# Optimization experiments

Hardware: AMD Instinct MI355X
Metric: run time of the kernel (lower is better)

## Reference

```python
import jax, jax.numpy as jnp
import numpy as np

H_DIM = 1024
N_HEADS = 16
HEAD_D = H_DIM // N_HEADS  # 64


def setup_inputs() -> dict:
    key = jax.random.key(0)
    ks = jax.random.split(key, 10)
    B, T, C = 2, 2048, H_DIM
    init = 1.0 / np.sqrt(C)  # lecun_normal-scale stand-in
    src = jax.random.normal(ks[0], (B, T, C), dtype=jnp.float32)
    mask = jnp.ones((B, T), dtype=jnp.float32)  # unused when causal
    Wq = jax.random.normal(ks[1], (C, H_DIM), dtype=jnp.float32) * init
    Wk = jax.random.normal(ks[2], (C, H_DIM), dtype=jnp.float32) * init
    Wv = jax.random.normal(ks[3], (C, H_DIM), dtype=jnp.float32) * init
    Wo = jax.random.normal(ks[4], (H_DIM, H_DIM), dtype=jnp.float32) * init
    bq = jnp.zeros((H_DIM,), jnp.float32)
    bk = jnp.zeros((H_DIM,), jnp.float32)
    bv = jnp.zeros((H_DIM,), jnp.float32)
    bo = jnp.zeros((H_DIM,), jnp.float32)
    return {"src": src, "mask": mask, "Wq": Wq, "bq": bq, "Wk": Wk, "bk": bk,
            "Wv": Wv, "bv": bv, "Wo": Wo, "bo": bo}


def reference(src, mask, Wq, bq, Wk, bk, Wv, bv, Wo, bo):
    # MaskedCausalAttention forward, deterministic=True (dropout = identity),
    # use_causal_mask=True.
    B, T, C = src.shape
    N, D = N_HEADS, HEAD_D
    # q,k,v: [B, N, T, D]
    q = (src @ Wq + bq).reshape(B, T, N, D).transpose(0, 2, 1, 3)
    k = (src @ Wk + bk).reshape(B, T, N, D).transpose(0, 2, 1, 3)
    v = (src @ Wv + bv).reshape(B, T, N, D).transpose(0, 2, 1, 3)
    # scores: [B, N, T, T]
    scores = jnp.einsum('bntd,bnsd->bnts', q, k) / jnp.sqrt(jnp.float32(D))
    causal = jnp.tril(jnp.ones((T, T), dtype=bool))[None, None]
    scores = jnp.where(causal, scores, -jnp.inf)
    probs = jax.nn.softmax(scores, axis=-1)
    attn = jnp.einsum('bnts,bnsd->bntd', probs, v)  # [B, N, T, D]
    attn = attn.transpose(0, 2, 1, 3).reshape(B, T, N * D)
    return attn @ Wo + bo
```

## Files before the change

kernel.cpp:

```cpp
#include <hip/hip_runtime.h>
#include <hip/hip_bf16.h>

typedef __hip_bfloat16 bf16;
typedef __attribute__((ext_vector_type(8))) short short8;
typedef __attribute__((ext_vector_type(4))) float f32x4;

#define BATCH 2
#define SEQ   2048
#define HDIM  1024
#define NHEAD 16
#define DHEAD 64
#define MROWS (BATCH*SEQ)

#define QSCALE 0.18033688f
#define EXP2F(x) __builtin_amdgcn_exp2f(x)

static __device__ __forceinline__ short f2bs(float x) {
    __hip_bfloat16 h = (__hip_bfloat16)x;
    return *reinterpret_cast<short*>(&h);
}
static __device__ __forceinline__ unsigned int pk2(float a, float b) {
    __hip_bfloat162 h = __float22bfloat162_rn(make_float2(a, b));
    return *reinterpret_cast<unsigned int*>(&h);
}

static __device__ __forceinline__ void gload16(const void* g, void* l) {
    __builtin_amdgcn_global_load_lds(
        (const __attribute__((address_space(1))) unsigned int*)g,
        (__attribute__((address_space(3))) unsigned int*)l, 16, 0, 0);
}

__global__ __launch_bounds__(256) void prep1(const float* __restrict__ src,
        const float* __restrict__ Wq, const float* __restrict__ Wk,
        const float* __restrict__ Wv,
        short* __restrict__ Sb, short* __restrict__ WqkT,
        short* __restrict__ WvT)
{
    __shared__ float t[64][65];
    const int bx = blockIdx.x, tid = threadIdx.x;
    if (bx < 4096) {
        int i = bx * 256 + tid;
        float4 v = ((const float4*)src)[i];
        ushort4 o;
        o.x = (unsigned short)f2bs(v.x);
        o.y = (unsigned short)f2bs(v.y);
        o.z = (unsigned short)f2bs(v.z);
        o.w = (unsigned short)f2bs(v.w);
        ((ushort4*)Sb)[i] = o;
        return;
    }
    const int tb = bx - 4096;
    const int wsel = tb >> 8;
    const float* W = (wsel == 0) ? Wq : (wsel == 1) ? Wk : Wv;
    short* dst = (wsel < 2) ? WqkT : WvT;
    const int roff = (wsel < 2) ? wsel * 1024 : 0;
    const int t8 = tb & 255;
    const int n0 = (t8 & 15) * 64, k0 = (t8 >> 4) * 64;
#pragma unroll
    for (int i = 0; i < 16; i++) {
        int idx = tid + i * 256, r = idx >> 6, c = idx & 63;
        t[r][c] = W[(size_t)(k0 + r) * HDIM + n0 + c];
    }
    __syncthreads();
#pragma unroll
    for (int i = 0; i < 16; i++) {
        int idx = tid + i * 256, c = idx >> 6, r = idx & 63;
        dst[(size_t)(roff + n0 + c) * HDIM + k0 + r] = f2bs(t[r][c]);
    }
}

__global__ __launch_bounds__(256) void gemm_qk(const short* __restrict__ A,
        const short* __restrict__ Bt,
        const float* __restrict__ bq, const float* __restrict__ bk,
        short* __restrict__ Qout, short* __restrict__ Kout)
{
    __shared__ short As[16 * 512];
    __shared__ short Bs[16 * 512];
    const int tid = threadIdx.x, lane = tid & 63, w = tid >> 6;
    const int quad = lane >> 4, l15 = lane & 15;
    const int m0 = blockIdx.y * 128, n0 = blockIdx.x * 128;
    const int wr = w >> 1, wc = w & 1;

    const short* gsrc[8];
    short* ldst[8];
#pragma unroll
    for (int i = 0; i < 8; i++) {
        int u = w * 8 + i;
        if (u < 16) {
            int mi = u >> 1, kh = u & 1;
            gsrc[i] = A + (size_t)(m0 + mi * 16 + l15) * HDIM + kh * 32 + quad * 8;
            ldst[i] = &As[u * 512];
        } else {
            int v = u - 16, ni = v >> 1, kh = v & 1;
            gsrc[i] = Bt + (size_t)(n0 + ni * 16 + l15) * HDIM + kh * 32 + quad * 8;
            ldst[i] = &Bs[v * 512];
        }
    }

    f32x4 acc[4][4];
#pragma unroll
    for (int i = 0; i < 4; i++)
#pragma unroll
        for (int j = 0; j < 4; j++) acc[i][j] = (f32x4){0.f, 0.f, 0.f, 0.f};

    for (int kk = 0; kk < 16; ++kk) {
        if (kk) __syncthreads();
#pragma unroll
        for (int i = 0; i < 8; i++) {
            gload16(gsrc[i], ldst[i]);
            gsrc[i] += 64;
        }
        __syncthreads();

#pragma unroll
        for (int kh = 0; kh < 2; kh++) {
            short8 af[4], bfr[4];
#pragma unroll
            for (int mi = 0; mi < 4; mi++)
                af[mi] = *(const short8*)&As[((wr * 4 + mi) * 2 + kh) * 512 + lane * 8];
#pragma unroll
            for (int ni = 0; ni < 4; ni++)
                bfr[ni] = *(const short8*)&Bs[((wc * 4 + ni) * 2 + kh) * 512 + lane * 8];
#pragma unroll
            for (int mi = 0; mi < 4; mi++)
#pragma unroll
                for (int ni = 0; ni < 4; ni++)
                    acc[mi][ni] = __builtin_amdgcn_mfma_f32_16x16x32_bf16(
                                      af[mi], bfr[ni], acc[mi][ni], 0, 0, 0);
        }
    }

    const int region = n0 >> 10;
    const float* bias = region ? bk : bq;
    const float oscale = region ? 1.0f : QSCALE;
    short* C = region ? Kout : Qout;

#pragma unroll
    for (int mi = 0; mi < 4; mi++) {
        int mB = m0 + (wr * 4 + mi) * 16 + quad * 4;
#pragma unroll
        for (int ni = 0; ni < 4; ni++) {
            int nl = (n0 + (wc * 4 + ni) * 16 + l15) & 1023;
            float bb = bias[nl];
#pragma unroll
            for (int r = 0; r < 4; r++)
                C[(size_t)(mB + r) * HDIM + nl] =
                    f2bs((acc[mi][ni][r] + bb) * oscale);
        }
    }
}

__global__ __launch_bounds__(256) void gemm_v(const short* __restrict__ A,
        const short* __restrict__ Bt, const float* __restrict__ bv,
        short* __restrict__ Vtout)
{
    __shared__ short As[8 * 512];
    __shared__ short Bs[16 * 512];
    const int tid = threadIdx.x, lane = tid & 63, w = tid >> 6;
    const int quad = lane >> 4, l15 = lane & 15;
    const int m0 = blockIdx.y * 64, n0 = blockIdx.x * 128;
    const int wr = w >> 1, wc = w & 1;

    const short* gsrc[6];
    short* ldst[6];
#pragma unroll
    for (int i = 0; i < 6; i++) {
        int u = w * 6 + i;
        if (u < 8) {
            int mi = u >> 1, kh = u & 1;
            gsrc[i] = A + (size_t)(m0 + mi * 16 + l15) * HDIM + kh * 32 + quad * 8;
            ldst[i] = &As[u * 512];
        } else {
            int v = u - 8, ni = v >> 1, kh = v & 1;
            gsrc[i] = Bt + (size_t)(n0 + ni * 16 + l15) * HDIM + kh * 32 + quad * 8;
            ldst[i] = &Bs[v * 512];
        }
    }

    f32x4 acc[2][4];
#pragma unroll
    for (int i = 0; i < 2; i++)
#pragma unroll
        for (int j = 0; j < 4; j++) acc[i][j] = (f32x4){0.f, 0.f, 0.f, 0.f};

    for (int kk = 0; kk < 16; ++kk) {
        if (kk) __syncthreads();
#pragma unroll
        for (int i = 0; i < 6; i++) {
            gload16(gsrc[i], ldst[i]);
            gsrc[i] += 64;
        }
        __syncthreads();

#pragma unroll
        for (int kh = 0; kh < 2; kh++) {
            short8 af[2], bfr[4];
#pragma unroll
            for (int mi = 0; mi < 2; mi++)
                af[mi] = *(const short8*)&As[((wr * 2 + mi) * 2 + kh) * 512 + lane * 8];
#pragma unroll
            for (int ni = 0; ni < 4; ni++)
                bfr[ni] = *(const short8*)&Bs[((wc * 4 + ni) * 2 + kh) * 512 + lane * 8];
#pragma unroll
            for (int mi = 0; mi < 2; mi++)
#pragma unroll
                for (int ni = 0; ni < 4; ni++)
                    acc[mi][ni] = __builtin_amdgcn_mfma_f32_16x16x32_bf16(
                                      af[mi], bfr[ni], acc[mi][ni], 0, 0, 0);
        }
    }

#pragma unroll
    for (int mi = 0; mi < 2; mi++) {
        int mB = m0 + (wr * 2 + mi) * 16 + quad * 4;
        int bb = mB >> 11, t = mB & 2047;
#pragma unroll
        for (int ni = 0; ni < 4; ni++) {
            int n = n0 + (wc * 4 + ni) * 16 + l15;
            int h = n >> 6, d = n & 63;
            float bvv = bv[n];
            size_t base = ((size_t)((bb * NHEAD + h) * DHEAD + d)) * SEQ + t;
            ushort4 pk;
            pk.x = (unsigned short)f2bs(acc[mi][ni][0] + bvv);
            pk.y = (unsigned short)f2bs(acc[mi][ni][1] + bvv);
            pk.z = (unsigned short)f2bs(acc[mi][ni][2] + bvv);
            pk.w = (unsigned short)f2bs(acc[mi][ni][3] + bvv);
            *(ushort4*)(Vtout + base) = pk;
        }
    }
}

__global__ __launch_bounds__(256) void gemm_o(const short* __restrict__ A,
        const short* __restrict__ Bt, const float* __restrict__ bo,
        float* __restrict__ Out)
{
    __shared__ short As[8 * 512];
    __shared__ short Bs[16 * 512];
    const int tid = threadIdx.x, lane = tid & 63, w = tid >> 6;
    const int quad = lane >> 4, l15 = lane & 15;
    const int m0 = blockIdx.y * 64, n0 = blockIdx.x * 128;
    const int wr = w >> 1, wc = w & 1;

    const short* gsrc[6];
    short* ldst[6];
#pragma unroll
    for (int i = 0; i < 6; i++) {
        int u = w * 6 + i;
        if (u < 8) {
            int mi = u >> 1, kh = u & 1;
            gsrc[i] = A + (size_t)(m0 + mi * 16 + l15) * HDIM + kh * 32 + quad * 8;
            ldst[i] = &As[u * 512];
        } else {
            int v = u - 8, ni = v >> 1, kh = v & 1;
            gsrc[i] = Bt + (size_t)(n0 + ni * 16 + l15) * HDIM + kh * 32 + quad * 8;
            ldst[i] = &Bs[v * 512];
        }
    }

    f32x4 acc[2][4];
#pragma unroll
    for (int i = 0; i < 2; i++)
#pragma unroll
        for (int j = 0; j < 4; j++) acc[i][j] = (f32x4){0.f, 0.f, 0.f, 0.f};

    for (int kk = 0; kk < 16; ++kk) {
        if (kk) __syncthreads();
#pragma unroll
        for (int i = 0; i < 6; i++) {
            gload16(gsrc[i], ldst[i]);
            gsrc[i] += 64;
        }
        __syncthreads();

#pragma unroll
        for (int kh = 0; kh < 2; kh++) {
            short8 af[2], bfr[4];
#pragma unroll
            for (int mi = 0; mi < 2; mi++)
                af[mi] = *(const short8*)&As[((wr * 2 + mi) * 2 + kh) * 512 + lane * 8];
#pragma unroll
            for (int ni = 0; ni < 4; ni++)
                bfr[ni] = *(const short8*)&Bs[((wc * 4 + ni) * 2 + kh) * 512 + lane * 8];
#pragma unroll
            for (int mi = 0; mi < 2; mi++)
#pragma unroll
                for (int ni = 0; ni < 4; ni++)
                    acc[mi][ni] = __builtin_amdgcn_mfma_f32_16x16x32_bf16(
                                      af[mi], bfr[ni], acc[mi][ni], 0, 0, 0);
        }
    }

#pragma unroll
    for (int mi = 0; mi < 2; mi++) {
        int mB = m0 + (wr * 2 + mi) * 16 + quad * 4;
#pragma unroll
        for (int ni = 0; ni < 4; ni++) {
            int n = n0 + (wc * 4 + ni) * 16 + l15;
            float bb = bo[n];
#pragma unroll
            for (int r = 0; r < 4; r++)
                Out[(size_t)(mB + r) * HDIM + n] = acc[mi][ni][r] + bb;
        }
    }
}

__global__ __launch_bounds__(256) void attn_mfma(const short* __restrict__ Qb,
        const short* __restrict__ Kb, const short* __restrict__ Vt,
        short* __restrict__ Ab,
        const float* __restrict__ Wo, short* __restrict__ WoT)
{
    __shared__ short SMEM[12800];
    short* Ks = SMEM;
    short* Vs = SMEM + 4096;
    short* Ps = SMEM + 8192;
    const int tid = threadIdx.x, lane = tid & 63, w = tid >> 6;
    const int quad = lane >> 4, l15 = lane & 15;
    const int L = blockIdx.x;

    if (L >= 1024) {
        float* t = (float*)SMEM;
        const int bsel = L - 1024;
#pragma unroll
        for (int j = 0; j < 8; j++) {
            int t8 = bsel * 8 + j;
            int n0 = (t8 & 15) * 64, k0 = (t8 >> 4) * 64;
            __syncthreads();
#pragma unroll
            for (int i = 0; i < 16; i++) {
                int idx = tid + i * 256, r = idx >> 6, c = idx & 63;
                t[r * 65 + c] = Wo[(size_t)(k0 + r) * HDIM + n0 + c];
            }
            __syncthreads();
#pragma unroll
            for (int i = 0; i < 16; i++) {
                int idx = tid + i * 256, c = idx >> 6, r = idx & 63;
                WoT[(size_t)(n0 + c) * HDIM + k0 + r] = f2bs(t[r * 65 + c]);
            }
        }
        return;
    }

    const int pair = (L & 7) + 8 * ((L >> 3) & 3);
    const int strip = 31 - (L >> 5);
    const int b = pair >> 4, head = pair & 15;

    const short* Kbh = Kb + (size_t)b * SEQ * HDIM + head * DHEAD;
    const short* Vth = Vt + (size_t)(b * NHEAD + head) * DHEAD * SEQ;
    short* Pw = &Ps[w * 1152];

    const int qbase = strip * 64;
    const int qr = qbase + w * 16 + l15;

    const short* qptr = Qb + (size_t)(b * SEQ + qr) * HDIM + head * DHEAD + quad * 8;
    short8 bq0 = *(const short8*)qptr;
    short8 bq1 = *(const short8*)(qptr + 32);

    f32x4 o[4];
#pragma unroll
    for (int dt = 0; dt < 4; dt++) o[dt] = (f32x4){0.f, 0.f, 0.f, 0.f};
    float psum = 0.f;

    for (int it = 0; it <= strip; ++it) {
        const int s0 = it * 64;
#pragma unroll
        for (int i = 0; i < 4; i++) {
            int u = w * 4 + i;
            if (u < 8) {
                int t = u >> 1, h = u & 1;
                gload16(Kbh + (size_t)(s0 + t * 16 + l15) * HDIM + h * 32 + quad * 8,
                        &Ks[u * 512]);
            } else {
                int c = u - 8, dt = c >> 1, kh = c & 1;
                gload16(Vth + (size_t)(dt * 16 + l15) * SEQ + s0 + kh * 32 + quad * 8,
                        &Vs[c * 512]);
            }
        }
        __syncthreads();

        f32x4 sv[4];
#pragma unroll
        for (int t = 0; t < 4; t++) {
            sv[t] = (f32x4){0.f, 0.f, 0.f, 0.f};
            short8 k0 = *(const short8*)&Ks[(t * 2) * 512 + lane * 8];
            short8 k1 = *(const short8*)&Ks[(t * 2 + 1) * 512 + lane * 8];
            sv[t] = __builtin_amdgcn_mfma_f32_16x16x32_bf16(k0, bq0, sv[t], 0, 0, 0);
            sv[t] = __builtin_amdgcn_mfma_f32_16x16x32_bf16(k1, bq1, sv[t], 0, 0, 0);
        }

        float p[16];
        if (it == strip) {
#pragma unroll
            for (int t = 0; t < 4; t++)
#pragma unroll
                for (int r = 0; r < 4; r++) {
                    int key = s0 + t * 16 + quad * 4 + r;
                    p[t * 4 + r] = (key <= qr) ? EXP2F(sv[t][r]) : 0.f;
                }
        } else {
#pragma unroll
            for (int t = 0; t < 4; t++)
#pragma unroll
                for (int r = 0; r < 4; r++)
                    p[t * 4 + r] = EXP2F(sv[t][r]);
        }
#pragma unroll
        for (int i = 0; i < 16; i++) psum += p[i];

#pragma unroll
        for (int t = 0; t < 4; t++) {
            uint2 u2;
            u2.x = pk2(p[t * 4],     p[t * 4 + 1]);
            u2.y = pk2(p[t * 4 + 2], p[t * 4 + 3]);
            *(uint2*)&Pw[l15 * 72 + t * 16 + quad * 4] = u2;
        }
        short8 bp0 = *(const short8*)&Pw[l15 * 72 + quad * 8];
        short8 bp1 = *(const short8*)&Pw[l15 * 72 + 32 + quad * 8];

#pragma unroll
        for (int dt = 0; dt < 4; dt++) {
            short8 av0 = *(const short8*)&Vs[(dt * 2) * 512 + lane * 8];
            short8 av1 = *(const short8*)&Vs[(dt * 2 + 1) * 512 + lane * 8];
            o[dt] = __builtin_amdgcn_mfma_f32_16x16x32_bf16(av0, bp0, o[dt], 0, 0, 0);
            o[dt] = __builtin_amdgcn_mfma_f32_16x16x32_bf16(av1, bp1, o[dt], 0, 0, 0);
        }
        __syncthreads();
    }

    float lrow = psum + __shfl_xor(psum, 16);
    lrow += __shfl_xor(lrow, 32);
    const float inv = 1.f / lrow;

    const size_t obase = (size_t)(b * SEQ + qr) * HDIM + head * DHEAD;
#pragma unroll
    for (int dt = 0; dt < 4; dt++) {
        uint2 u2;
        u2.x = pk2(o[dt][0] * inv, o[dt][1] * inv);
        u2.y = pk2(o[dt][2] * inv, o[dt][3] * inv);
        *(uint2*)&Ab[obase + dt * 16 + quad * 4] = u2;
    }
}

extern "C" void kernel_launch(void* const* d_in, const int* in_sizes, int n_in,
                              void* d_out, int out_size, void* d_ws, size_t ws_size,
                              hipStream_t stream)
{
    const float* src = (const float*)d_in[0];
    const float* Wq = (const float*)d_in[2];
    const float* bq = (const float*)d_in[3];
    const float* Wk = (const float*)d_in[4];
    const float* bk = (const float*)d_in[5];
    const float* Wv = (const float*)d_in[6];
    const float* bv = (const float*)d_in[7];
    const float* Wo = (const float*)d_in[8];
    const float* bo = (const float*)d_in[9];
    float* out = (float*)d_out;

    short* Sb   = (short*)d_ws;
    short* Qb   = Sb + (size_t)MROWS * HDIM;
    short* Kb   = Qb + (size_t)MROWS * HDIM;
    short* Vt   = Kb + (size_t)MROWS * HDIM;
    short* slot = Vt + (size_t)MROWS * HDIM;
    short* WqkT = Vt;
    short* Ab   = Qb;

    dim3 blk(256);

    prep1<<<dim3(4096 + 768), blk, 0, stream>>>(src, Wq, Wk, Wv, Sb, WqkT, slot);

    gemm_qk<<<dim3(16, 32), blk, 0, stream>>>(Sb, WqkT, bq, bk, Qb, Kb);

    gemm_v<<<dim3(8, 64), blk, 0, stream>>>(Sb, slot, bv, Vt);

    attn_mfma<<<dim3(1024 + 32), blk, 0, stream>>>(Qb, Kb, Vt, Ab, Wo, slot);

    gemm_o<<<dim3(8, 64), blk, 0, stream>>>(Ab, slot, bo, out);
}
```

Before: 224.7 us.

## Fuse QKV projection, move Wo transpose to prep, double-buffer attention K/V loads

Measured after the change: 224.7 us. Within noise of the previous version (-0.0%).

```diff
diff --git a/kernel.cpp b/kernel.cpp
--- a/kernel.cpp
+++ b/kernel.cpp
@@ -32,9 +32,9 @@
 
 __global__ __launch_bounds__(256) void prep1(const float* __restrict__ src,
         const float* __restrict__ Wq, const float* __restrict__ Wk,
-        const float* __restrict__ Wv,
-        short* __restrict__ Sb, short* __restrict__ WqkT,
-        short* __restrict__ WvT)
+        const float* __restrict__ Wv, const float* __restrict__ Wo,
+        short* __restrict__ Sb, short* __restrict__ WT,
+        short* __restrict__ WoT)
 {
     __shared__ float t[64][65];
     const int bx = blockIdx.x, tid = threadIdx.x;
@@ -51,9 +51,9 @@
     }
     const int tb = bx - 4096;
     const int wsel = tb >> 8;
-    const float* W = (wsel == 0) ? Wq : (wsel == 1) ? Wk : Wv;
-    short* dst = (wsel < 2) ? WqkT : WvT;
-    const int roff = (wsel < 2) ? wsel * 1024 : 0;
+    const float* W = (wsel == 0) ? Wq : (wsel == 1) ? Wk : (wsel == 2) ? Wv : Wo;
+    short* dst = (wsel < 3) ? WT : WoT;
+    const int roff = (wsel < 3) ? wsel * 1024 : 0;
     const int t8 = tb & 255;
     const int n0 = (t8 & 15) * 64, k0 = (t8 >> 4) * 64;
 #pragma unroll
@@ -69,10 +69,12 @@
     }
 }
 
-__global__ __launch_bounds__(256) void gemm_qk(const short* __restrict__ A,
+__global__ __launch_bounds__(256) void gemm_qkv(const short* __restrict__ A,
         const short* __restrict__ Bt,
         const float* __restrict__ bq, const float* __restrict__ bk,
-        short* __restrict__ Qout, short* __restrict__ Kout)
+        const float* __restrict__ bv,
+        short* __restrict__ Qout, short* __restrict__ Kout,
+        short* __restrict__ Vtout)
 {
     __shared__ short As[16 * 512];
     __shared__ short Bs[16 * 512];
@@ -131,28 +133,179 @@
     }
 
     const int region = n0 >> 10;
-    const float* bias = region ? bk : bq;
-    const float oscale = region ? 1.0f : QSCALE;
-    short* C = region ? Kout : Qout;
-
-#pragma unroll
-    for (int mi = 0; mi < 4; mi++) {
-        int mB = m0 + (wr * 4 + mi) * 16 + quad * 4;
-#pragma unroll
-        for (int ni = 0; ni < 4; ni++) {
-            int nl = (n0 + (wc * 4 + ni) * 16 + l15) & 1023;
-            float bb = bias[nl];
-#pragma unroll
-            for (int r = 0; r < 4; r++)
-                C[(size_t)(mB + r) * HDIM + nl] =
-                    f2bs((acc[mi][ni][r] + bb) * oscale);
-        }
-    }
-}
-
-__global__ __launch_bounds__(256) void gemm_v(const short* __restrict__ A,
-        const short* __restrict__ Bt, const float* __restrict__ bv,
-        short* __restrict__ Vtout)
+    if (region < 2) {
+        const float* bias = region ? bk : bq;
+        const float oscale = region ? 1.0f : QSCALE;
+        short* C = region ? Kout : Qout;
+#pragma unroll
+        for (int mi = 0; mi < 4; mi++) {
+            int mB = m0 + (wr * 4 + mi) * 16 + quad * 4;
+#pragma unroll
+            for (int ni = 0; ni < 4; ni++) {
+                int nl = (n0 + (wc * 4 + ni) * 16 + l15) & 1023;
+                float bb = bias[nl];
+#pragma unroll
+                for (int r = 0; r < 4; r++)
+                    C[(size_t)(mB + r) * HDIM + nl] =
+                        f2bs((acc[mi][ni][r] + bb) * oscale);
+            }
+        }
+    } else {
+#pragma unroll
+        for (int mi = 0; mi < 4; mi++) {
+            int mB = m0 + (wr * 4 + mi) * 16 + quad * 4;
+            int bb = mB >> 11, t = mB & 2047;
+#pragma unroll
+            for (int ni = 0; ni < 4; ni++) {
+                int n = n0 + (wc * 4 + ni) * 16 + l15;
+                int h = (n >> 6) & 15, d = n & 63;
+                float bvv = bv[n & 1023];
+                size_t base = ((size_t)((bb * NHEAD + h) * DHEAD + d)) * SEQ + t;
+                ushort4 pk;
+                pk.x = (unsigned short)f2bs(acc[mi][ni][0] + bvv);
+                pk.y = (unsigned short)f2bs(acc[mi][ni][1] + bvv);
+                pk.z = (unsigned short)f2bs(acc[mi][ni][2] + bvv);
+                pk.w = (unsigned short)f2bs(acc[mi][ni][3] + bvv);
+                *(ushort4*)(Vtout + base) = pk;
+            }
+        }
+    }
+}
+
+__global__ __launch_bounds__(256) void attn_mfma(const short* __restrict__ Qb,
+        const short* __restrict__ Kb, const short* __restrict__ Vt,
+        short* __restrict__ Ab)
+{
+    __shared__ short SMEM[20992];
+    const int tid = threadIdx.x, lane = tid & 63, w = tid >> 6;
+    const int quad = lane >> 4, l15 = lane & 15;
+    const int L = blockIdx.x;
+
+    const int pair = (L & 7) + 8 * ((L >> 3) & 3);
+    const int strip = 31 - (L >> 5);
+    const int b = pair >> 4, head = pair & 15;
+
+    const short* Kbh = Kb + (size_t)b * SEQ * HDIM + head * DHEAD;
+    const short* Vth = Vt + (size_t)(b * NHEAD + head) * DHEAD * SEQ;
+    short* Pw = SMEM + 16384 + w * 1152;
+
+    const int qbase = strip * 64;
+    const int qr = qbase + w * 16 + l15;
+
+    const short* qptr = Qb + (size_t)(b * SEQ + qr) * HDIM + head * DHEAD + quad * 8;
+    short8 bq0 = *(const short8*)qptr;
+    short8 bq1 = *(const short8*)(qptr + 32);
+
+    const short* gp[4];
+    int stp[4], ldo[4];
+#pragma unroll
+    for (int i = 0; i < 4; i++) {
+        int u = w * 4 + i;
+        if (u < 8) {
+            int t = u >> 1, h = u & 1;
+            gp[i] = Kbh + (size_t)(t * 16 + l15) * HDIM + h * 32 + quad * 8;
+            stp[i] = 64 * HDIM;
+        } else {
+            int c = u - 8, dt = c >> 1, kh = c & 1;
+            gp[i] = Vth + (size_t)(dt * 16 + l15) * SEQ + kh * 32 + quad * 8;
+            stp[i] = 64;
+        }
+        ldo[i] = u * 512;
+    }
+
+    f32x4 o[4];
+#pragma unroll
+    for (int dt = 0; dt < 4; dt++) o[dt] = (f32x4){0.f, 0.f, 0.f, 0.f};
+    float psum = 0.f;
+
+#pragma unroll
+    for (int i = 0; i < 4; i++) { gload16(gp[i], &SMEM[ldo[i]]); gp[i] += stp[i]; }
+
+    for (int it = 0; it <= strip; ++it) {
+        const int cur = it & 1;
+        short* Ks = &SMEM[cur * 8192];
+        short* Vs = Ks + 4096;
+
+        if (it < strip) {
+            short* nb = &SMEM[(cur ^ 1) * 8192];
+#pragma unroll
+            for (int i = 0; i < 4; i++) { gload16(gp[i], nb + ldo[i]); gp[i] += stp[i]; }
+            asm volatile("s_waitcnt vmcnt(4)" ::: "memory");
+        } else {
+            asm volatile("s_waitcnt vmcnt(0)" ::: "memory");
+        }
+        __builtin_amdgcn_s_barrier();
+        const int s0 = it * 64;
+        f32x4 sv[4];
+        __builtin_amdgcn_s_setprio(1);
+#pragma unroll
+        for (int t = 0; t < 4; t++) {
+            sv[t] = (f32x4){0.f, 0.f, 0.f, 0.f};
+            short8 k0 = *(const short8*)&Ks[(t * 2) * 512 + lane * 8];
+            short8 k1 = *(const short8*)&Ks[(t * 2 + 1) * 512 + lane * 8];
+            sv[t] = __builtin_amdgcn_mfma_f32_16x16x32_bf16(k0, bq0, sv[t], 0, 0, 0);
+            sv[t] = __builtin_amdgcn_mfma_f32_16x16x32_bf16(k1, bq1, sv[t], 0, 0, 0);
+        }
+        __builtin_amdgcn_s_setprio(0);
+
+        float p[16];
+        if (it == strip) {
+#pragma unroll
+            for (int t = 0; t < 4; t++)
+#pragma unroll
+                for (int r = 0; r < 4; r++) {
+                    int key = s0 + t * 16 + quad * 4 + r;
+                    p[t * 4 + r] = (key <= qr) ? EXP2F(sv[t][r]) : 0.f;
+                }
+        } else {
+#pragma unroll
+            for (int t = 0; t < 4; t++)
+#pragma unroll
+                for (int r = 0; r < 4; r++)
+                    p[t * 4 + r] = EXP2F(sv[t][r]);
+        }
+#pragma unroll
+        for (int i = 0; i < 16; i++) psum += p[i];
+
+#pragma unroll
+        for (int t = 0; t < 4; t++) {
+            uint2 u2;
+            u2.x = pk2(p[t * 4],     p[t * 4 + 1]);
+            u2.y = pk2(p[t * 4 + 2], p[t * 4 + 3]);
+            *(uint2*)&Pw[l15 * 72 + t * 16 + quad * 4] = u2;
+        }
+        short8 bp0 = *(const short8*)&Pw[l15 * 72 + quad * 8];
+        short8 bp1 = *(const short8*)&Pw[l15 * 72 + 32 + quad * 8];
+
+        __builtin_amdgcn_s_setprio(1);
+#pragma unroll
+        for (int dt = 0; dt < 4; dt++) {
+            short8 av0 = *(const short8*)&Vs[(dt * 2) * 512 + lane * 8];
+            short8 av1 = *(const short8*)&Vs[(dt * 2 + 1) * 512 + lane * 8];
+            o[dt] = __builtin_amdgcn_mfma_f32_16x16x32_bf16(av0, bp0, o[dt], 0, 0, 0);
+            o[dt] = __builtin_amdgcn_mfma_f32_16x16x32_bf16(av1, bp1, o[dt], 0, 0, 0);
+        }
+        __builtin_amdgcn_s_setprio(0);
+        __builtin_amdgcn_s_barrier();
+    }
+
+    float lrow = psum + __shfl_xor(psum, 16);
+    lrow += __shfl_xor(lrow, 32);
+    const float inv = 1.f / lrow;
+
+    const size_t obase = (size_t)(b * SEQ + qr) * HDIM + head * DHEAD;
+#pragma unroll
+    for (int dt = 0; dt < 4; dt++) {
+        uint2 u2;
+        u2.x = pk2(o[dt][0] * inv, o[dt][1] * inv);
+        u2.y = pk2(o[dt][2] * inv, o[dt][3] * inv);
+        *(uint2*)&Ab[obase + dt * 16 + quad * 4] = u2;
+    }
+}
+
+__global__ __launch_bounds__(256) void gemm_o(const short* __restrict__ A,
+        const short* __restrict__ Bt, const float* __restrict__ bo,
+        float* __restrict__ Out)
 {
     __shared__ short As[8 * 512];
     __shared__ short Bs[16 * 512];
@@ -213,86 +366,6 @@
 #pragma unroll
     for (int mi = 0; mi < 2; mi++) {
         int mB = m0 + (wr * 2 + mi) * 16 + quad * 4;
-        int bb = mB >> 11, t = mB & 2047;
-#pragma unroll
-        for (int ni = 0; ni < 4; ni++) {
-            int n = n0 + (wc * 4 + ni) * 16 + l15;
-            int h = n >> 6, d = n & 63;
-            float bvv = bv[n];
-            size_t base = ((size_t)((bb * NHEAD + h) * DHEAD + d)) * SEQ + t;
-            ushort4 pk;
-            pk.x = (unsigned short)f2bs(acc[mi][ni][0] + bvv);
-            pk.y = (unsigned short)f2bs(acc[mi][ni][1] + bvv);
-            pk.z = (unsigned short)f2bs(acc[mi][ni][2] + bvv);
-            pk.w = (unsigned short)f2bs(acc[mi][ni][3] + bvv);
-            *(ushort4*)(Vtout + base) = pk;
-        }
-    }
-}
-
-__global__ __launch_bounds__(256) void gemm_o(const short* __restrict__ A,
-        const short* __restrict__ Bt, const float* __restrict__ bo,
-        float* __restrict__ Out)
-{
-    __shared__ short As[8 * 512];
-    __shared__ short Bs[16 * 512];
-    const int tid = threadIdx.x, lane = tid & 63, w = tid >> 6;
-    const int quad = lane >> 4, l15 = lane & 15;
-    const int m0 = blockIdx.y * 64, n0 = blockIdx.x * 128;
-    const int wr = w >> 1, wc = w & 1;
-
-    const short* gsrc[6];
-    short* ldst[6];
-#pragma unroll
-    for (int i = 0; i < 6; i++) {
-        int u = w * 6 + i;
-        if (u < 8) {
-            int mi = u >> 1, kh = u & 1;
-            gsrc[i] = A + (size_t)(m0 + mi * 16 + l15) * HDIM + kh * 32 + quad * 8;
-            ldst[i] = &As[u * 512];
-        } else {
-            int v = u - 8, ni = v >> 1, kh = v & 1;
-            gsrc[i] = Bt + (size_t)(n0 + ni * 16 + l15) * HDIM + kh * 32 + quad * 8;
-            ldst[i] = &Bs[v * 512];
-        }
-    }
-
-    f32x4 acc[2][4];
-#pragma unroll
-    for (int i = 0; i < 2; i++)
-#pragma unroll
-        for (int j = 0; j < 4; j++) acc[i][j] = (f32x4){0.f, 0.f, 0.f, 0.f};
-
-    for (int kk = 0; kk < 16; ++kk) {
-        if (kk) __syncthreads();
-#pragma unroll
-        for (int i = 0; i < 6; i++) {
-            gload16(gsrc[i], ldst[i]);
-            gsrc[i] += 64;
-        }
-        __syncthreads();
-
-#pragma unroll
-        for (int kh = 0; kh < 2; kh++) {
-            short8 af[2], bfr[4];
-#pragma unroll
-            for (int mi = 0; mi < 2; mi++)
-                af[mi] = *(const short8*)&As[((wr * 2 + mi) * 2 + kh) * 512 + lane * 8];
-#pragma unroll
-            for (int ni = 0; ni < 4; ni++)
-                bfr[ni] = *(const short8*)&Bs[((wc * 4 + ni) * 2 + kh) * 512 + lane * 8];
-#pragma unroll
-            for (int mi = 0; mi < 2; mi++)
-#pragma unroll
-                for (int ni = 0; ni < 4; ni++)
-                    acc[mi][ni] = __builtin_amdgcn_mfma_f32_16x16x32_bf16(
-                                      af[mi], bfr[ni], acc[mi][ni], 0, 0, 0);
-        }
-    }
-
-#pragma unroll
-    for (int mi = 0; mi < 2; mi++) {
-        int mB = m0 + (wr * 2 + mi) * 16 + quad * 4;
 #pragma unroll
         for (int ni = 0; ni < 4; ni++) {
             int n = n0 + (wc * 4 + ni) * 16 + l15;
@@ -301,142 +374,6 @@
             for (int r = 0; r < 4; r++)
                 Out[(size_t)(mB + r) * HDIM + n] = acc[mi][ni][r] + bb;
         }
-    }
-}
-
-__global__ __launch_bounds__(256) void attn_mfma(const short* __restrict__ Qb,
-        const short* __restrict__ Kb, const short* __restrict__ Vt,
-        short* __restrict__ Ab,
-        const float* __restrict__ Wo, short* __restrict__ WoT)
-{
-    __shared__ short SMEM[12800];
-    short* Ks = SMEM;
-    short* Vs = SMEM + 4096;
-    short* Ps = SMEM + 8192;
-    const int tid = threadIdx.x, lane = tid & 63, w = tid >> 6;
-    const int quad = lane >> 4, l15 = lane & 15;
-    const int L = blockIdx.x;
-
-    if (L >= 1024) {
-        float* t = (float*)SMEM;
-        const int bsel = L - 1024;
-#pragma unroll
-        for (int j = 0; j < 8; j++) {
-            int t8 = bsel * 8 + j;
-            int n0 = (t8 & 15) * 64, k0 = (t8 >> 4) * 64;
-            __syncthreads();
-#pragma unroll
-            for (int i = 0; i < 16; i++) {
-                int idx = tid + i * 256, r = idx >> 6, c = idx & 63;
-                t[r * 65 + c] = Wo[(size_t)(k0 + r) * HDIM + n0 + c];
-            }
-            __syncthreads();
-#pragma unroll
-            for (int i = 0; i < 16; i++) {
-                int idx = tid + i * 256, c = idx >> 6, r = idx & 63;
-                WoT[(size_t)(n0 + c) * HDIM + k0 + r] = f2bs(t[r * 65 + c]);
-            }
-        }
-        return;
-    }
-
-    const int pair = (L & 7) + 8 * ((L >> 3) & 3);
-    const int strip = 31 - (L >> 5);
-    const int b = pair >> 4, head = pair & 15;
-
-    const short* Kbh = Kb + (size_t)b * SEQ * HDIM + head * DHEAD;
-    const short* Vth = Vt + (size_t)(b * NHEAD + head) * DHEAD * SEQ;
-    short* Pw = &Ps[w * 1152];
-
-    const int qbase = strip * 64;
-    const int qr = qbase + w * 16 + l15;
-
-    const short* qptr = Qb + (size_t)(b * SEQ + qr) * HDIM + head * DHEAD + quad * 8;
-    short8 bq0 = *(const short8*)qptr;
-    short8 bq1 = *(const short8*)(qptr + 32);
-
-    f32x4 o[4];
-#pragma unroll
-    for (int dt = 0; dt < 4; dt++) o[dt] = (f32x4){0.f, 0.f, 0.f, 0.f};
-    float psum = 0.f;
-
-    for (int it = 0; it <= strip; ++it) {
-        const int s0 = it * 64;
-#pragma unroll
-        for (int i = 0; i < 4; i++) {
-            int u = w * 4 + i;
-            if (u < 8) {
-                int t = u >> 1, h = u & 1;
-                gload16(Kbh + (size_t)(s0 + t * 16 + l15) * HDIM + h * 32 + quad * 8,
-                        &Ks[u * 512]);
-            } else {
-                int c = u - 8, dt = c >> 1, kh = c & 1;
-                gload16(Vth + (size_t)(dt * 16 + l15) * SEQ + s0 + kh * 32 + quad * 8,
-                        &Vs[c * 512]);
-            }
-        }
-        __syncthreads();
-
-        f32x4 sv[4];
-#pragma unroll
-        for (int t = 0; t < 4; t++) {
-            sv[t] = (f32x4){0.f, 0.f, 0.f, 0.f};
-            short8 k0 = *(const short8*)&Ks[(t * 2) * 512 + lane * 8];
-            short8 k1 = *(const short8*)&Ks[(t * 2 + 1) * 512 + lane * 8];
-            sv[t] = __builtin_amdgcn_mfma_f32_16x16x32_bf16(k0, bq0, sv[t], 0, 0, 0);
-            sv[t] = __builtin_amdgcn_mfma_f32_16x16x32_bf16(k1, bq1, sv[t], 0, 0, 0);
-        }
-
-        float p[16];
-        if (it == strip) {
-#pragma unroll
-            for (int t = 0; t < 4; t++)
-#pragma unroll
-                for (int r = 0; r < 4; r++) {
-                    int key = s0 + t * 16 + quad * 4 + r;
-                    p[t * 4 + r] = (key <= qr) ? EXP2F(sv[t][r]) : 0.f;
-                }
-        } else {
-#pragma unroll
-            for (int t = 0; t < 4; t++)
-#pragma unroll
-                for (int r = 0; r < 4; r++)
-                    p[t * 4 + r] = EXP2F(sv[t][r]);
-        }
-#pragma unroll
-        for (int i = 0; i < 16; i++) psum += p[i];
-
-#pragma unroll
-        for (int t = 0; t < 4; t++) {
-            uint2 u2;
-            u2.x = pk2(p[t * 4],     p[t * 4 + 1]);
-            u2.y = pk2(p[t * 4 + 2], p[t * 4 + 3]);
-            *(uint2*)&Pw[l15 * 72 + t * 16 + quad * 4] = u2;
-        }
-        short8 bp0 = *(const short8*)&Pw[l15 * 72 + quad * 8];
-        short8 bp1 = *(const short8*)&Pw[l15 * 72 + 32 + quad * 8];
-
-#pragma unroll
-        for (int dt = 0; dt < 4; dt++) {
-            short8 av0 = *(const short8*)&Vs[(dt * 2) * 512 + lane * 8];
-            short8 av1 = *(const short8*)&Vs[(dt * 2 + 1) * 512 + lane * 8];
-            o[dt] = __builtin_amdgcn_mfma_f32_16x16x32_bf16(av0, bp0, o[dt], 0, 0, 0);
-            o[dt] = __builtin_amdgcn_mfma_f32_16x16x32_bf16(av1, bp1, o[dt], 0, 0, 0);
-        }
-        __syncthreads();
-    }
-
-    float lrow = psum + __shfl_xor(psum, 16);
-    lrow += __shfl_xor(lrow, 32);
-    const float inv = 1.f / lrow;
-
-    const size_t obase = (size_t)(b * SEQ + qr) * HDIM + head * DHEAD;
-#pragma unroll
-    for (int dt = 0; dt < 4; dt++) {
-        uint2 u2;
-        u2.x = pk2(o[dt][0] * inv, o[dt][1] * inv);
-        u2.y = pk2(o[dt][2] * inv, o[dt][3] * inv);
-        *(uint2*)&Ab[obase + dt * 16 + quad * 4] = u2;
     }
 }
 
@@ -459,19 +396,17 @@
     short* Qb   = Sb + (size_t)MROWS * HDIM;
     short* Kb   = Qb + (size_t)MROWS * HDIM;
     short* Vt   = Kb + (size_t)MROWS * HDIM;
-    short* slot = Vt + (size_t)MROWS * HDIM;
-    short* WqkT = Vt;
+    short* WoT  = Vt + (size_t)MROWS * HDIM;
+    short* WT   = (short*)d_out;
     short* Ab   = Qb;
 
     dim3 blk(256);
 
-    prep1<<<dim3(4096 + 768), blk, 0, stream>>>(src, Wq, Wk, Wv, Sb, WqkT, slot);
-
-    gemm_qk<<<dim3(16, 32), blk, 0, stream>>>(Sb, WqkT, bq, bk, Qb, Kb);
-
-    gemm_v<<<dim3(8, 64), blk, 0, stream>>>(Sb, slot, bv, Vt);
-
-    attn_mfma<<<dim3(1024 + 32), blk, 0, stream>>>(Qb, Kb, Vt, Ab, Wo, slot);
-
-    gemm_o<<<dim3(8, 64), blk, 0, stream>>>(Ab, slot, bo, out);
-}
+    prep1<<<dim3(4096 + 1024), blk, 0, stream>>>(src, Wq, Wk, Wv, Wo, Sb, WT, WoT);
+
+    gemm_qkv<<<dim3(24, 32), blk, 0, stream>>>(Sb, WT, bq, bk, bv, Qb, Kb, Vt);
+
+    attn_mfma<<<dim3(1024), blk, 0, stream>>>(Qb, Kb, Vt, Ab);
+
+    gemm_o<<<dim3(8, 64), blk, 0, stream>>>(Ab, WoT, bo, out);
+}
```
